# Performance work log

Hardware: AMD Instinct MI355X
Metric: run time of the kernel (lower is better)

Reference implementation:

```python
import jax, jax.numpy as jnp
import numpy as np

N_VISIBLE = 50000
N_HIDDEN = 5000
N_NODES = N_VISIBLE + N_HIDDEN
N_EDGES = 1_000_000
BATCH = 128


def setup_inputs() -> dict:
    key = jax.random.key(0)
    k1, k2, k3, k4, k5 = jax.random.split(key, 5)
    # parameters, initialized as in the torch module
    linear = 0.05 * (2.0 * jax.random.uniform(k1, (N_NODES,), dtype=jnp.float32) - 1.0)
    quadratic = 5.0 * (2.0 * jax.random.uniform(k2, (N_EDGES,), dtype=jnp.float32) - 1.0)
    # bipartite visible-hidden edges -> CSR-like flat buffers (via segment ids)
    flat_adj = jax.random.randint(k3, (N_EDGES,), 0, N_VISIBLE, dtype=jnp.int32).astype(jnp.int64)  # visible endpoint per edge
    seg_ids = jax.random.randint(k4, (N_EDGES,), 0, N_HIDDEN, dtype=jnp.int32).astype(jnp.int64)    # hidden bin per edge
    flat_j_idx = jnp.arange(N_EDGES, dtype=jnp.int64)  # quadratic coefficient index per flat entry
    hidden_idx = jnp.arange(N_HIDDEN, dtype=jnp.int64) + N_VISIBLE
    # observed spin configurations in {0,1} (mapped to +-1 inside reference)
    s = jax.random.randint(k5, (BATCH, N_NODES), 0, 2, dtype=jnp.int32)
    return {
        "linear": linear,
        "quadratic": quadratic,
        "s": s,
        "flat_adj": flat_adj,
        "flat_j_idx": flat_j_idx,
        "seg_ids": seg_ids,
        "hidden_idx": hidden_idx,
        "n_hidden": N_HIDDEN,
    }


def reference(linear, quadratic, s, flat_adj, flat_j_idx, seg_ids, hidden_idx, n_hidden):
    """Per-hidden-unit effective field + conditional spin expectation.

    eff[b, k] = linear[hidden_idx[k]]
                + sum_{e : seg_ids[e]==k} quadratic[flat_j_idx[e]] * s_pm[b, flat_adj[e]]
    returns tanh(-eff)  (conditional expectation of hidden spins given visibles)
    """
    s_pm = (2 * s - 1).astype(linear.dtype)                 # {0,1} -> {-1,+1}, (B, N)
    w = quadratic[flat_j_idx]                               # (E,)
    contrib = s_pm[:, flat_adj].T * w[:, None]              # (E, B) gathered neighbor terms
    field = jax.ops.segment_sum(contrib, seg_ids, num_segments=n_hidden)  # (K, B)
    eff = field.T + linear[hidden_idx][None, :]             # (B, K)
    return jnp.tanh(-eff)
```

## Files before the change

kernel.cpp:

```cpp
#include <hip/hip_runtime.h>
#include <math.h>
#include <stdint.h>

#define NV 50000
#define NH 5000
#define NN 55000
#define NCB 313
#define BCAP 4096
#define KSLOT 384
#define CHUNK 4096


__device__ __forceinline__ uint32_t selmask(uint32_t word, uint32_t bsh) {
    return (uint32_t)((int32_t)(word << (31u - bsh)) >> 31);
}

__global__ void __launch_bounds__(256) pack_zero_kernel(
        const int* __restrict__ s, uint32_t* __restrict__ bits,
        uint32_t* __restrict__ coarse_cnt) {
    if (blockIdx.x == 0)
        for (int i = threadIdx.x; i < NCB; i += 256) coarse_cnt[i] = 0u;
    int tid = blockIdx.x * 256 + threadIdx.x;
    int v = tid >> 2;
    int g = tid & 3;
    if (v >= NV) return;
    const int* col = s + (size_t)g * 32 * NN + v;
    uint32_t w = 0;
#pragma unroll
    for (int j = 0; j < 32; ++j)
        w |= (uint32_t)(col[(size_t)j * NN] & 1) << j;
    bits[(size_t)v * 4 + g] = w;
}

__global__ void __launch_bounds__(256) coarse_split_kernel(
        const int4* __restrict__ seg4, const int4* __restrict__ adj4,
        const float4* __restrict__ quad4,
        uint32_t* __restrict__ coarse_cnt, uint2* __restrict__ recs, int E) {
    __shared__ uint32_t hist[320];
    __shared__ uint32_t loc[320];
    __shared__ uint32_t cur[NCB];
    __shared__ uint32_t gbase[NCB];
    __shared__ __align__(16) uint2 st[CHUNK];
    __shared__ uint32_t dst[CHUNK];
    const int tid = threadIdx.x;
    for (int i = tid; i < 320; i += 256) hist[i] = 0u;
    __syncthreads();

    const int c0 = blockIdx.x * CHUNK;
    const int nloc = min(CHUNK, E - c0);
    int kreg[16];
#pragma unroll
    for (int j = 0; j < 4; ++j) {
        int t4 = (c0 >> 2) + j * 256 + tid;
        bool ok = t4 < ((c0 + nloc) >> 2);
        int4 sg = ok ? seg4[t4] : make_int4(-1, -1, -1, -1);
        kreg[j * 4 + 0] = sg.x; kreg[j * 4 + 1] = sg.y;
        kreg[j * 4 + 2] = sg.z; kreg[j * 4 + 3] = sg.w;
        if (ok) {
            atomicAdd(&hist[sg.x >> 4], 1u);
            atomicAdd(&hist[sg.y >> 4], 1u);
            atomicAdd(&hist[sg.z >> 4], 1u);
            atomicAdd(&hist[sg.w >> 4], 1u);
        }
    }
    __syncthreads();
    for (int i = tid; i < NCB; i += 256)
        gbase[i] = atomicAdd(&coarse_cnt[i], hist[i]);
    for (int i = tid; i < 320; i += 256) loc[i] = hist[i];
    __syncthreads();
    for (int d = 1; d < 320; d <<= 1) {
        uint32_t v0 = 0, v1 = 0;
        int i1 = tid + 256;
        if (tid >= d) v0 = loc[tid - d];
        if (i1 < 320 && i1 >= d) v1 = loc[i1 - d];
        __syncthreads();
        if (tid >= d) loc[tid] += v0;
        if (i1 < 320 && i1 >= d) loc[i1] += v1;
        __syncthreads();
    }
    for (int i = tid; i < NCB; i += 256) cur[i] = loc[i] - hist[i];
    __syncthreads();
#pragma unroll
    for (int j = 0; j < 4; ++j) {
        int t4 = (c0 >> 2) + j * 256 + tid;
        if (t4 < ((c0 + nloc) >> 2)) {
            int4 a = adj4[t4];
            float4 q = quad4[t4];
#pragma unroll
            for (int cmp = 0; cmp < 4; ++cmp) {
                int k = kreg[j * 4 + cmp];
                int v = (cmp == 0) ? a.x : (cmp == 1) ? a.y : (cmp == 2) ? a.z : a.w;
                float w = (cmp == 0) ? q.x : (cmp == 1) ? q.y : (cmp == 2) ? q.z : q.w;
                int bk = k >> 4;
                uint32_t slot = atomicAdd(&cur[bk], 1u);
                uint32_t rank = gbase[bk] + (slot - (loc[bk] - hist[bk]));
                st[slot] = make_uint2((uint32_t)v | ((uint32_t)(k & 15) << 16),
                                      __float_as_uint(w));
                dst[slot] = (rank < BCAP) ? (uint32_t)bk * BCAP + rank : ~0u;
            }
        }
    }
    __syncthreads();
    for (int i = tid; i < nloc; i += 256) {
        uint32_t d = dst[i];
        if (d != ~0u) recs[d] = st[i];
    }
}

__global__ void __launch_bounds__(256) quarter_field_kernel(
        const uint32_t* __restrict__ coarse_cnt, const uint2* __restrict__ recs,
        const uint4* __restrict__ bits4, const float* __restrict__ linear,
        float* __restrict__ out) {
    const int x = blockIdx.x;
    const int j = (x & 7) * 157 + (x >> 3);
    const int bkt = j >> 2;
    const int q = j & 3;
    if (bkt >= NCB) return;
    const int tid = threadIdx.x;

    __shared__ uint32_t cur4[4];
    __shared__ float swp[4];
    __shared__ __align__(16) uint32_t rows[4][5][KSLOT];
    __shared__ float part[4][256];

    if (tid < 4) cur4[tid] = 0u;
    else if (tid < 8) swp[tid - 4] = 0.f;
    __syncthreads();

    int cnt = (int)min(coarse_cnt[bkt], (uint32_t)BCAP);
    const uint4* region4 = (const uint4*)(recs + (size_t)bkt * BCAP);
    float sw0 = 0.f, sw1 = 0.f, sw2 = 0.f, sw3 = 0.f;
    for (int i2 = tid; i2 * 2 < cnt; i2 += 256) {
        uint4 rr = region4[i2];
#pragma unroll
        for (int h = 0; h < 2; ++h) {
            int idx = i2 * 2 + h;
            if (idx >= cnt) break;
            uint32_t rx = h ? rr.z : rr.x;
            uint32_t ry = h ? rr.w : rr.y;
            int kl = (int)((rx >> 16) & 15u);
            if ((kl >> 2) == q) {
                int l = kl & 3;
                uint32_t p = atomicAdd(&cur4[l], 1u);
                if (p < KSLOT) {
                    uint4 mw = bits4[rx & 0xFFFFu];
                    rows[l][0][p] = mw.x;
                    rows[l][1][p] = mw.y;
                    rows[l][2][p] = mw.z;
                    rows[l][3][p] = mw.w;
                    rows[l][4][p] = ry;
                    float wv = __uint_as_float(ry);
                    if (l == 0) sw0 += wv;
                    else if (l == 1) sw1 += wv;
                    else if (l == 2) sw2 += wv;
                    else sw3 += wv;
                }
            }
        }
    }
#pragma unroll
    for (int off = 32; off; off >>= 1) {
        sw0 += __shfl_down(sw0, off);
        sw1 += __shfl_down(sw1, off);
        sw2 += __shfl_down(sw2, off);
        sw3 += __shfl_down(sw3, off);
    }
    if ((tid & 63) == 0) {
        atomicAdd(&swp[0], sw0);
        atomicAdd(&swp[1], sw1);
        atomicAdd(&swp[2], sw2);
        atomicAdd(&swp[3], sw3);
    }
    __syncthreads();

    if (tid < 4) {
        int c = min((int)cur4[tid], KSLOT);
        int T8 = (c + 7) & ~7;
        for (int t = c; t < T8; ++t) rows[tid][4][t] = 0u;
        cur4[tid] = (uint32_t)T8;
    }
    __syncthreads();

    const int b = tid & 127;
    const int grp = tid >> 7;
    const uint32_t bsh = (uint32_t)(b & 31);
    const int widx = b >> 5;
#pragma unroll
    for (int kk = 0; kk < 4; ++kk) {
        int T8 = (int)cur4[kk];
        const uint32_t* mrow = rows[kk][widx];
        const uint32_t* wrow = rows[kk][4];
        float a0 = 0.f, a1 = 0.f, a2 = 0.f, a3 = 0.f;
        for (int i = grp * 4; i < T8; i += 8) {
            uint4 mm = *(const uint4*)(mrow + i);
            uint4 ww = *(const uint4*)(wrow + i);
            a0 += __uint_as_float(ww.x & selmask(mm.x, bsh));
            a1 += __uint_as_float(ww.y & selmask(mm.y, bsh));
            a2 += __uint_as_float(ww.z & selmask(mm.z, bsh));
            a3 += __uint_as_float(ww.w & selmask(mm.w, bsh));
        }
        part[kk][tid] = (a0 + a1) + (a2 + a3);
    }
    __syncthreads();

    if (tid < 128) {
        int k0 = bkt * 16 + q * 4;
        if (k0 + 3 < NH) {
            float4 o;
            float* op = (float*)&o;
#pragma unroll
            for (int kk = 0; kk < 4; ++kk) {
                float acc = part[kk][tid] + part[kk][tid + 128];
                float e = 2.f * acc - swp[kk] + linear[NV + k0 + kk];
                op[kk] = tanhf(-e);
            }
            *(float4*)(out + (size_t)tid * NH + k0) = o;
        }
    }
}

extern "C" void kernel_launch(void* const* d_in, const int* in_sizes, int n_in,
                              void* d_out, int out_size, void* d_ws, size_t ws_size,
                              hipStream_t stream) {
    const float* linear = (const float*)d_in[0];
    const float* quad   = (const float*)d_in[1];
    const int*   s      = (const int*)d_in[2];
    const int*   adj    = (const int*)d_in[3];
    const int*   seg    = (const int*)d_in[5];
    const int E = in_sizes[5];
    float* out = (float*)d_out;

    char* ws = (char*)d_ws;
    uint32_t* bits       = (uint32_t*)(ws);
    uint32_t* coarse_cnt = (uint32_t*)(ws + 800000);
    uint2*    recs       = (uint2*)   (ws + 801280);

    pack_zero_kernel<<<(NV * 4 + 255) / 256, 256, 0, stream>>>(s, bits, coarse_cnt);
    const int nchunk = (E + CHUNK - 1) / CHUNK;
    coarse_split_kernel<<<nchunk, 256, 0, stream>>>(
        (const int4*)seg, (const int4*)adj, (const float4*)quad, coarse_cnt, recs, E);
    quarter_field_kernel<<<1256, 256, 0, stream>>>(coarse_cnt, recs, (const uint4*)bits,
                                                   linear, out);
}
```

Measured before the change: 142.1 us.

## Stage records then gather bit rows per wave; compute two batch lanes per thread via sign flip

The filter pass now only stores each matching (index, weight) record into shared memory. A second pass, one wave per hidden unit, gathers the packed spin words and fills the padded rows, which decouples the random global gathers from the atomic slot assignment. The dot-product loop now covers two batch lanes per thread by flipping the weight's sign bit from the spin bit. This removes the separate weight-sum reduction and the 2*acc - sum correction. The cost is an extra shared staging buffer, a four-way final reduction, and a larger shared-memory footprint that may lower occupancy.

```diff
diff --git a/kernel.cpp b/kernel.cpp
--- a/kernel.cpp
+++ b/kernel.cpp
@@ -8,12 +8,9 @@
 #define NCB 313
 #define BCAP 4096
 #define KSLOT 384
+#define KPAD 388
 #define CHUNK 4096
 
-
-__device__ __forceinline__ uint32_t selmask(uint32_t word, uint32_t bsh) {
-    return (uint32_t)((int32_t)(word << (31u - bsh)) >> 31);
-}
 
 __global__ void __launch_bounds__(256) pack_zero_kernel(
         const int* __restrict__ s, uint32_t* __restrict__ bits,
@@ -119,17 +116,15 @@
     const int tid = threadIdx.x;
 
     __shared__ uint32_t cur4[4];
-    __shared__ float swp[4];
-    __shared__ __align__(16) uint32_t rows[4][5][KSLOT];
-    __shared__ float part[4][256];
+    __shared__ __align__(16) uint2 st4[4][KSLOT];
+    __shared__ __align__(16) uint32_t rows[4][5][KPAD];
+    __shared__ float part[4][256][2];
 
     if (tid < 4) cur4[tid] = 0u;
-    else if (tid < 8) swp[tid - 4] = 0.f;
     __syncthreads();
 
     int cnt = (int)min(coarse_cnt[bkt], (uint32_t)BCAP);
     const uint4* region4 = (const uint4*)(recs + (size_t)bkt * BCAP);
-    float sw0 = 0.f, sw1 = 0.f, sw2 = 0.f, sw3 = 0.f;
     for (int i2 = tid; i2 * 2 < cnt; i2 += 256) {
         uint4 rr = region4[i2];
 #pragma unroll
@@ -142,79 +137,78 @@
             if ((kl >> 2) == q) {
                 int l = kl & 3;
                 uint32_t p = atomicAdd(&cur4[l], 1u);
-                if (p < KSLOT) {
-                    uint4 mw = bits4[rx & 0xFFFFu];
-                    rows[l][0][p] = mw.x;
-                    rows[l][1][p] = mw.y;
-                    rows[l][2][p] = mw.z;
-                    rows[l][3][p] = mw.w;
-                    rows[l][4][p] = ry;
-                    float wv = __uint_as_float(ry);
-                    if (l == 0) sw0 += wv;
-                    else if (l == 1) sw1 += wv;
-                    else if (l == 2) sw2 += wv;
-                    else sw3 += wv;
-                }
+                if (p < KSLOT) st4[l][p] = make_uint2(rx, ry);
             }
         }
     }
-#pragma unroll
-    for (int off = 32; off; off >>= 1) {
-        sw0 += __shfl_down(sw0, off);
-        sw1 += __shfl_down(sw1, off);
-        sw2 += __shfl_down(sw2, off);
-        sw3 += __shfl_down(sw3, off);
-    }
-    if ((tid & 63) == 0) {
-        atomicAdd(&swp[0], sw0);
-        atomicAdd(&swp[1], sw1);
-        atomicAdd(&swp[2], sw2);
-        atomicAdd(&swp[3], sw3);
-    }
-    __syncthreads();
-
-    if (tid < 4) {
-        int c = min((int)cur4[tid], KSLOT);
-        int T8 = (c + 7) & ~7;
-        for (int t = c; t < T8; ++t) rows[tid][4][t] = 0u;
-        cur4[tid] = (uint32_t)T8;
-    }
-    __syncthreads();
-
-    const int b = tid & 127;
-    const int grp = tid >> 7;
-    const uint32_t bsh = (uint32_t)(b & 31);
-    const int widx = b >> 5;
+    __syncthreads();
+
+    {
+        const int w = tid >> 6;
+        const int lane = tid & 63;
+        int c = min((int)cur4[w], KSLOT);
+        int T16 = (c + 15) & ~15;
+        for (int t = c + lane; t < T16; t += 64) rows[w][4][t] = 0u;
+        for (int t = lane; t < c; t += 64) {
+            uint2 r = st4[w][t];
+            uint4 mw = bits4[r.x & 0xFFFFu];
+            rows[w][0][t] = mw.x;
+            rows[w][1][t] = mw.y;
+            rows[w][2][t] = mw.z;
+            rows[w][3][t] = mw.w;
+            rows[w][4][t] = r.y;
+        }
+        if (lane == 0) cur4[w] = (uint32_t)T16;
+    }
+    __syncthreads();
+
+    const int grp  = tid >> 6;
+    const int pair = tid & 63;
+    const int bl   = pair & 15;
+    const int widx = pair >> 4;
+    const uint32_t sh0 = (uint32_t)(31 - bl);
+    const uint32_t sh1 = (uint32_t)(15 - bl);
 #pragma unroll
     for (int kk = 0; kk < 4; ++kk) {
-        int T8 = (int)cur4[kk];
-        const uint32_t* mrow = rows[kk][widx];
-        const uint32_t* wrow = rows[kk][4];
-        float a0 = 0.f, a1 = 0.f, a2 = 0.f, a3 = 0.f;
-        for (int i = grp * 4; i < T8; i += 8) {
+        int T16 = (int)cur4[kk];
+        const uint32_t* mrow = &rows[kk][widx][0];
+        const uint32_t* wrow = &rows[kk][4][0];
+        float a0 = 0.f, b0 = 0.f, a1 = 0.f, b1 = 0.f;
+        for (int i = grp * 4; i < T16; i += 16) {
             uint4 mm = *(const uint4*)(mrow + i);
             uint4 ww = *(const uint4*)(wrow + i);
-            a0 += __uint_as_float(ww.x & selmask(mm.x, bsh));
-            a1 += __uint_as_float(ww.y & selmask(mm.y, bsh));
-            a2 += __uint_as_float(ww.z & selmask(mm.z, bsh));
-            a3 += __uint_as_float(ww.w & selmask(mm.w, bsh));
-        }
-        part[kk][tid] = (a0 + a1) + (a2 + a3);
+            uint32_t n0 = ~mm.x, n1 = ~mm.y, n2 = ~mm.z, n3 = ~mm.w;
+            a0 += __uint_as_float(ww.x ^ ((n0 << sh0) & 0x80000000u));
+            a1 += __uint_as_float(ww.x ^ ((n0 << sh1) & 0x80000000u));
+            b0 += __uint_as_float(ww.y ^ ((n1 << sh0) & 0x80000000u));
+            b1 += __uint_as_float(ww.y ^ ((n1 << sh1) & 0x80000000u));
+            a0 += __uint_as_float(ww.z ^ ((n2 << sh0) & 0x80000000u));
+            a1 += __uint_as_float(ww.z ^ ((n2 << sh1) & 0x80000000u));
+            b0 += __uint_as_float(ww.w ^ ((n3 << sh0) & 0x80000000u));
+            b1 += __uint_as_float(ww.w ^ ((n3 << sh1) & 0x80000000u));
+        }
+        part[kk][tid][0] = a0 + b0;
+        part[kk][tid][1] = a1 + b1;
     }
     __syncthreads();
 
     if (tid < 128) {
+        int b = tid;
+        int bl31 = b & 31;
+        int p = (b >> 5) * 16 + (bl31 & 15);
+        int slot = bl31 >> 4;
         int k0 = bkt * 16 + q * 4;
         if (k0 + 3 < NH) {
             float4 o;
             float* op = (float*)&o;
 #pragma unroll
             for (int kk = 0; kk < 4; ++kk) {
-                float acc = part[kk][tid] + part[kk][tid + 128];
-                float e = 2.f * acc - swp[kk] + linear[NV + k0 + kk];
+                float acc = part[kk][p][slot] + part[kk][64 + p][slot]
+                          + part[kk][128 + p][slot] + part[kk][192 + p][slot];
+                float e = acc + linear[NV + k0 + kk];
                 op[kk] = tanhf(-e);
             }
-            *(float4*)(out + (size_t)tid * NH + k0) = o;
+            *(float4*)(out + (size_t)b * NH + k0) = o;
         }
     }
 }
```

Measured after the change: 139.6 us. No clear change (-1.8%).

## Bucket edges per 4 hidden units so field blocks read only their records

Applied to the files above, without the earlier changes.

The split kernel now bins edges into 1252 buckets of 4 hidden units instead of 313 buckets of 16. Each field block therefore reads only its own edges rather than scanning a 16-unit bucket and discarding three quarters of it. The local prefix scan is rebuilt as a per-thread 5-element serial scan plus a 256-wide block scan, and the per-record destination array is replaced by recomputing the destination from the stored bucket id during scatter. The finer bucketing adds histogram and global atomic work and a larger scan in the split kernel, and lowers the per-bucket cap to 1024 records.

```diff
diff --git a/kernel.cpp b/kernel.cpp
--- a/kernel.cpp
+++ b/kernel.cpp
@@ -5,8 +5,9 @@
 #define NV 50000
 #define NH 5000
 #define NN 55000
-#define NCB 313
-#define BCAP 4096
+#define NB4 1252
+#define NBP 1280
+#define BCAP 1024
 #define KSLOT 384
 #define CHUNK 4096
 
@@ -19,7 +20,7 @@
         const int* __restrict__ s, uint32_t* __restrict__ bits,
         uint32_t* __restrict__ coarse_cnt) {
     if (blockIdx.x == 0)
-        for (int i = threadIdx.x; i < NCB; i += 256) coarse_cnt[i] = 0u;
+        for (int i = threadIdx.x; i < NBP; i += 256) coarse_cnt[i] = 0u;
     int tid = blockIdx.x * 256 + threadIdx.x;
     int v = tid >> 2;
     int g = tid & 3;
@@ -36,14 +37,14 @@
         const int4* __restrict__ seg4, const int4* __restrict__ adj4,
         const float4* __restrict__ quad4,
         uint32_t* __restrict__ coarse_cnt, uint2* __restrict__ recs, int E) {
-    __shared__ uint32_t hist[320];
-    __shared__ uint32_t loc[320];
-    __shared__ uint32_t cur[NCB];
-    __shared__ uint32_t gbase[NCB];
+    __shared__ uint32_t hist[NBP];
+    __shared__ uint32_t locex[NBP];
+    __shared__ uint32_t cur[NBP];
+    __shared__ uint32_t gbase[NBP];
+    __shared__ uint32_t wsum[256];
     __shared__ __align__(16) uint2 st[CHUNK];
-    __shared__ uint32_t dst[CHUNK];
     const int tid = threadIdx.x;
-    for (int i = tid; i < 320; i += 256) hist[i] = 0u;
+    for (int i = tid; i < NBP; i += 256) hist[i] = 0u;
     __syncthreads();
 
     const int c0 = blockIdx.x * CHUNK;
@@ -57,28 +58,35 @@
         kreg[j * 4 + 0] = sg.x; kreg[j * 4 + 1] = sg.y;
         kreg[j * 4 + 2] = sg.z; kreg[j * 4 + 3] = sg.w;
         if (ok) {
-            atomicAdd(&hist[sg.x >> 4], 1u);
-            atomicAdd(&hist[sg.y >> 4], 1u);
-            atomicAdd(&hist[sg.z >> 4], 1u);
-            atomicAdd(&hist[sg.w >> 4], 1u);
-        }
-    }
-    __syncthreads();
-    for (int i = tid; i < NCB; i += 256)
+            atomicAdd(&hist[sg.x >> 2], 1u);
+            atomicAdd(&hist[sg.y >> 2], 1u);
+            atomicAdd(&hist[sg.z >> 2], 1u);
+            atomicAdd(&hist[sg.w >> 2], 1u);
+        }
+    }
+    __syncthreads();
+    for (int i = tid; i < NB4; i += 256)
         gbase[i] = atomicAdd(&coarse_cnt[i], hist[i]);
-    for (int i = tid; i < 320; i += 256) loc[i] = hist[i];
-    __syncthreads();
-    for (int d = 1; d < 320; d <<= 1) {
-        uint32_t v0 = 0, v1 = 0;
-        int i1 = tid + 256;
-        if (tid >= d) v0 = loc[tid - d];
-        if (i1 < 320 && i1 >= d) v1 = loc[i1 - d];
+    uint32_t hh[5];
+    {
+        int base = tid * 5;
+        uint32_t tot = 0;
+#pragma unroll
+        for (int t = 0; t < 5; ++t) { hh[t] = hist[base + t]; tot += hh[t]; }
+        wsum[tid] = tot;
         __syncthreads();
-        if (tid >= d) loc[tid] += v0;
-        if (i1 < 320 && i1 >= d) loc[i1] += v1;
-        __syncthreads();
-    }
-    for (int i = tid; i < NCB; i += 256) cur[i] = loc[i] - hist[i];
+        for (int d = 1; d < 256; d <<= 1) {
+            uint32_t v = (tid >= d) ? wsum[tid - d] : 0u;
+            __syncthreads();
+            wsum[tid] += v;
+            __syncthreads();
+        }
+        uint32_t off = wsum[tid] - tot;
+#pragma unroll
+        for (int t = 0; t < 5; ++t) { locex[base + t] = off; off += hh[t]; }
+    }
+    __syncthreads();
+    for (int i = tid; i < NBP; i += 256) cur[i] = locex[i];
     __syncthreads();
 #pragma unroll
     for (int j = 0; j < 4; ++j) {
@@ -91,31 +99,28 @@
                 int k = kreg[j * 4 + cmp];
                 int v = (cmp == 0) ? a.x : (cmp == 1) ? a.y : (cmp == 2) ? a.z : a.w;
                 float w = (cmp == 0) ? q.x : (cmp == 1) ? q.y : (cmp == 2) ? q.z : q.w;
-                int bk = k >> 4;
-                uint32_t slot = atomicAdd(&cur[bk], 1u);
-                uint32_t rank = gbase[bk] + (slot - (loc[bk] - hist[bk]));
-                st[slot] = make_uint2((uint32_t)v | ((uint32_t)(k & 15) << 16),
+                uint32_t slot = atomicAdd(&cur[k >> 2], 1u);
+                st[slot] = make_uint2((uint32_t)v | ((uint32_t)k << 16),
                                       __float_as_uint(w));
-                dst[slot] = (rank < BCAP) ? (uint32_t)bk * BCAP + rank : ~0u;
             }
         }
     }
     __syncthreads();
     for (int i = tid; i < nloc; i += 256) {
-        uint32_t d = dst[i];
-        if (d != ~0u) recs[d] = st[i];
-    }
-}
-
-__global__ void __launch_bounds__(256) quarter_field_kernel(
+        uint2 r = st[i];
+        uint32_t b = r.x >> 18;
+        uint32_t rank = gbase[b] + ((uint32_t)i - locex[b]);
+        if (rank < BCAP) recs[(size_t)b * BCAP + rank] = r;
+    }
+}
+
+__global__ void __launch_bounds__(256) field_kernel(
         const uint32_t* __restrict__ coarse_cnt, const uint2* __restrict__ recs,
         const uint4* __restrict__ bits4, const float* __restrict__ linear,
         float* __restrict__ out) {
     const int x = blockIdx.x;
-    const int j = (x & 7) * 157 + (x >> 3);
-    const int bkt = j >> 2;
-    const int q = j & 3;
-    if (bkt >= NCB) return;
+    const int bkt = (x & 7) * 157 + (x >> 3);
+    if (bkt >= NB4) return;
     const int tid = threadIdx.x;
 
     __shared__ uint32_t cur4[4];
@@ -123,39 +128,28 @@
     __shared__ __align__(16) uint32_t rows[4][5][KSLOT];
     __shared__ float part[4][256];
 
-    if (tid < 4) cur4[tid] = 0u;
-    else if (tid < 8) swp[tid - 4] = 0.f;
-    __syncthreads();
-
-    int cnt = (int)min(coarse_cnt[bkt], (uint32_t)BCAP);
-    const uint4* region4 = (const uint4*)(recs + (size_t)bkt * BCAP);
+    if (tid < 4) { cur4[tid] = 0u; swp[tid] = 0.f; }
+    __syncthreads();
+
+    int cnt = min((int)coarse_cnt[bkt], BCAP);
+    const uint2* region = recs + (size_t)bkt * BCAP;
     float sw0 = 0.f, sw1 = 0.f, sw2 = 0.f, sw3 = 0.f;
-    for (int i2 = tid; i2 * 2 < cnt; i2 += 256) {
-        uint4 rr = region4[i2];
-#pragma unroll
-        for (int h = 0; h < 2; ++h) {
-            int idx = i2 * 2 + h;
-            if (idx >= cnt) break;
-            uint32_t rx = h ? rr.z : rr.x;
-            uint32_t ry = h ? rr.w : rr.y;
-            int kl = (int)((rx >> 16) & 15u);
-            if ((kl >> 2) == q) {
-                int l = kl & 3;
-                uint32_t p = atomicAdd(&cur4[l], 1u);
-                if (p < KSLOT) {
-                    uint4 mw = bits4[rx & 0xFFFFu];
-                    rows[l][0][p] = mw.x;
-                    rows[l][1][p] = mw.y;
-                    rows[l][2][p] = mw.z;
-                    rows[l][3][p] = mw.w;
-                    rows[l][4][p] = ry;
-                    float wv = __uint_as_float(ry);
-                    if (l == 0) sw0 += wv;
-                    else if (l == 1) sw1 += wv;
-                    else if (l == 2) sw2 += wv;
-                    else sw3 += wv;
-                }
-            }
+    for (int i = tid; i < cnt; i += 256) {
+        uint2 r = region[i];
+        int l = (int)((r.x >> 16) & 3u);
+        uint4 mw = bits4[r.x & 0xFFFFu];
+        uint32_t p = atomicAdd(&cur4[l], 1u);
+        if (p < KSLOT) {
+            rows[l][0][p] = mw.x;
+            rows[l][1][p] = mw.y;
+            rows[l][2][p] = mw.z;
+            rows[l][3][p] = mw.w;
+            rows[l][4][p] = r.y;
+            float wv = __uint_as_float(r.y);
+            if (l == 0) sw0 += wv;
+            else if (l == 1) sw1 += wv;
+            else if (l == 2) sw2 += wv;
+            else sw3 += wv;
         }
     }
 #pragma unroll
@@ -172,7 +166,6 @@
         atomicAdd(&swp[3], sw3);
     }
     __syncthreads();
-
     if (tid < 4) {
         int c = min((int)cur4[tid], KSLOT);
         int T8 = (c + 7) & ~7;
@@ -188,8 +181,8 @@
 #pragma unroll
     for (int kk = 0; kk < 4; ++kk) {
         int T8 = (int)cur4[kk];
-        const uint32_t* mrow = rows[kk][widx];
-        const uint32_t* wrow = rows[kk][4];
+        const uint32_t* mrow = &rows[kk][widx][0];
+        const uint32_t* wrow = &rows[kk][4][0];
         float a0 = 0.f, a1 = 0.f, a2 = 0.f, a3 = 0.f;
         for (int i = grp * 4; i < T8; i += 8) {
             uint4 mm = *(const uint4*)(mrow + i);
@@ -204,7 +197,7 @@
     __syncthreads();
 
     if (tid < 128) {
-        int k0 = bkt * 16 + q * 4;
+        int k0 = bkt * 4;
         if (k0 + 3 < NH) {
             float4 o;
             float* op = (float*)&o;
@@ -233,12 +226,12 @@
     char* ws = (char*)d_ws;
     uint32_t* bits       = (uint32_t*)(ws);
     uint32_t* coarse_cnt = (uint32_t*)(ws + 800000);
-    uint2*    recs       = (uint2*)   (ws + 801280);
+    uint2*    recs       = (uint2*)   (ws + 805376);
 
     pack_zero_kernel<<<(NV * 4 + 255) / 256, 256, 0, stream>>>(s, bits, coarse_cnt);
     const int nchunk = (E + CHUNK - 1) / CHUNK;
     coarse_split_kernel<<<nchunk, 256, 0, stream>>>(
         (const int4*)seg, (const int4*)adj, (const float4*)quad, coarse_cnt, recs, E);
-    quarter_field_kernel<<<1256, 256, 0, stream>>>(coarse_cnt, recs, (const uint4*)bits,
-                                                   linear, out);
-}
+    field_kernel<<<1256, 256, 0, stream>>>(coarse_cnt, recs, (const uint4*)bits,
+                                           linear, out);
+}
```

Result: slower. 145.2 us (+2.2%).
